# Performance work log

Measured on AMD Instinct MI355X. Metric: run time of the kernel, lower is better.

The kernel has to match this reference:

```python
import math
import jax, jax.numpy as jnp
import numpy as np

N_HEADS = 8
FACTOR = 1


def setup_inputs() -> dict:
    key = jax.random.key(0)
    ks = jax.random.split(key, 8)
    B, L, D = 8, 2048, 512
    scale = 0.05
    return {
        "queries": jax.random.normal(ks[0], (B, L, D), jnp.float32),
        "keys": jax.random.normal(ks[1], (B, L, D), jnp.float32),
        "values": jax.random.normal(ks[2], (B, L, D), jnp.float32),
        "Wq": jax.random.normal(ks[3], (D, D), jnp.float32) * scale,
        "bq": jnp.zeros((D,), jnp.float32),
        "Wk": jax.random.normal(ks[4], (D, D), jnp.float32) * scale,
        "bk": jnp.zeros((D,), jnp.float32),
        "Wv": jax.random.normal(ks[5], (D, D), jnp.float32) * scale,
        "bv": jnp.zeros((D,), jnp.float32),
        "Wo": jax.random.normal(ks[6], (D, D), jnp.float32) * scale,
        "bo": jnp.zeros((D,), jnp.float32),
    }


def _autocorrelation(q, k, v):
    # q,k,v: [B, L, H, E]; L == S assumed (as built in setup_inputs)
    B, L, H, E = q.shape
    qp = jnp.transpose(q, (0, 2, 3, 1))  # [B,H,E,L]
    kp = jnp.transpose(k, (0, 2, 3, 1))
    vp = jnp.transpose(v, (0, 2, 3, 1))
    q_fft = jnp.fft.rfft(qp, axis=-1)
    k_fft = jnp.fft.rfft(kp, axis=-1)
    corr = jnp.fft.irfft(q_fft * jnp.conj(k_fft), n=L, axis=-1)  # [B,H,E,L]

    # training-path time-delay aggregation
    top_k = int(FACTOR * math.log(L))  # static python int
    mean_value = corr.mean(axis=(1, 2))  # [B, L]
    _, index = jax.lax.top_k(mean_value.mean(axis=0), top_k)  # [K] global delays
    weights = mean_value[:, index]  # [B, K]
    tmp_corr = jax.nn.softmax(weights, axis=-1)  # [B, K]
    # roll(v, -d) along last axis == gather at (t + d) mod L
    idx = (jnp.arange(L)[None, :] + index[:, None]) % L  # [K, L]
    patterns = vp[..., idx]  # [B,H,E,K,L]
    delays_agg = jnp.einsum('bhekl,bk->bhel', patterns, tmp_corr)  # [B,H,E,L]
    return jnp.transpose(delays_agg, (0, 3, 1, 2))  # [B,L,H,E]


def reference(queries, keys, values, Wq, bq, Wk, bk, Wv, bv, Wo, bo):
    B, L, Dm = queries.shape
    H = N_HEADS
    q = (queries @ Wq + bq).reshape(B, L, H, -1)
    k = (keys @ Wk + bk).reshape(B, L, H, -1)
    v = (values @ Wv + bv).reshape(B, L, H, -1)
    out = _autocorrelation(q, k, v).reshape(B, L, -1)
    return out @ Wo + bo
```

## Files before the change

kernel.cpp:

```cpp
#include <hip/hip_runtime.h>
#include <stdint.h>

#define BATCH 8
#define L_SEQ 2048
#define D_MODEL 512
#define TOPK 7
#define BM 128
#define BN 128
#define BK 32
#define LT 136

typedef _Float16 f16x8 __attribute__((ext_vector_type(8)));
typedef __attribute__((ext_vector_type(4))) float f32x4;
typedef unsigned short u16;
typedef unsigned int u32;

__device__ __forceinline__ u16 f2h(float f) {
    union { _Float16 h; u16 u; } v; v.h = (_Float16)f; return v.u;
}

__device__ __forceinline__ void load_lds16(const u16* g, u16* l) {
    __builtin_amdgcn_global_load_lds(
        (const __attribute__((address_space(1))) u32*)(g),
        (__attribute__((address_space(3))) u32*)(l), 16, 0, 0);
}


__global__ __launch_bounds__(256, 3) void gemm_qkv(
    const float* __restrict__ Xq, const float* __restrict__ Xk, const float* __restrict__ Xv,
    const u16* __restrict__ Wqt, const u16* __restrict__ Wkt, const u16* __restrict__ Wvt,
    const float* __restrict__ bq, const float* __restrict__ bk, const float* __restrict__ bv,
    u16* __restrict__ QT, u16* __restrict__ KT, u16* __restrict__ Vout)
{
    __shared__ __align__(16) u16 smem[2 * BM * 32 + 2 * BN * BK];
    u16* lT = smem;
    u16* lBb = smem + 2 * BM * 32;

    const int tid = threadIdx.x;
    const int hw = blockIdx.x;
    const int lg = (hw & 7) * 192 + (hw >> 3);
    const int bn = lg & 3, bm = (lg >> 2) & 127, z = lg >> 9;

    const int lane = tid & 63, wave = tid >> 6;
    const int wm = wave >> 1, wn = wave & 1;
    const int l15 = lane & 15, quad = lane >> 4;

    const float* A  = (z == 0) ? Xq  : (z == 1) ? Xk  : Xv;
    const u16*   Bt = (z == 0) ? Wqt : (z == 1) ? Wkt : Wvt;
    const float* bias = (z == 0) ? bq : (z == 1) ? bk : bv;

    const int s0 = wave * 64 + lane, s1 = s0 + 256;
    const int r0 = s0 >> 2, c0 = (s0 & 3) ^ ((r0 >> 1) & 3);
    const int r1 = s1 >> 2, c1 = (s1 & 3) ^ ((r1 >> 1) & 3);
    const u16* gB0 = Bt + (long)(bn * BN + r0) * D_MODEL + c0 * 8;
    const u16* gB1 = Bt + (long)(bn * BN + r1) * D_MODEL + c1 * 8;

    f32x4 acc[4][4] = {};

    {
        load_lds16(gB0, lBb + wave * 512);
        load_lds16(gB1, lBb + 2048 + wave * 512);
        gB0 += BK; gB1 += BK;
        #pragma unroll
        for (int j = 0; j < 4; ++j) {
            int idx = tid + j * 256;
            int row = idx >> 3, c4 = (idx & 7) * 4;
            int cs = (((c4 >> 3) ^ (row & 3)) << 3) | (c4 & 7);
            float4 va = *(const float4*)(A + (long)(bm * BM + row) * D_MODEL + c4);
            ushort4 pa;
            pa.x = f2h(va.x); pa.y = f2h(va.y); pa.z = f2h(va.z); pa.w = f2h(va.w);
            *(ushort4*)&smem[row * 32 + cs] = pa;
        }
    }
    __syncthreads();

    for (int t = 0; t < 16; ++t) {
        const int cur = t & 1;
        u16* lAc = smem + cur * (BM * 32);
        u16* lBc = lBb + cur * (BN * BK);
        u16* lAn = smem + (cur ^ 1) * (BM * 32);
        u16* lBn = lBb + (cur ^ 1) * (BN * BK);
        const bool nx = (t < 15);
        const int k1 = (t + 1) * BK;

        float4 va[4];
        if (nx) {
            load_lds16(gB0, lBn + wave * 512);
            load_lds16(gB1, lBn + 2048 + wave * 512);
            gB0 += BK; gB1 += BK;
            #pragma unroll
            for (int j = 0; j < 4; ++j) {
                int idx = tid + j * 256;
                int row = idx >> 3, c4 = (idx & 7) * 4;
                va[j] = *(const float4*)(A + (long)(bm * BM + row) * D_MODEL + k1 + c4);
            }
        }

        f16x8 fa[4], fb[4];
        #pragma unroll
        for (int i = 0; i < 4; ++i) {
            int r = wm * 64 + i * 16 + l15;
            fa[i] = *(const f16x8*)&lAc[r * 32 + ((quad ^ (r & 3)) << 3)];
        }
        #pragma unroll
        for (int j = 0; j < 4; ++j) {
            int n = wn * 64 + j * 16 + l15;
            int cs = quad ^ ((n >> 1) & 3);
            fb[j] = *(const f16x8*)&lBc[n * 32 + cs * 8];
        }
        #pragma unroll
        for (int i = 0; i < 4; ++i)
            #pragma unroll
            for (int j = 0; j < 4; ++j)
                acc[i][j] = __builtin_amdgcn_mfma_f32_16x16x32_f16(fa[i], fb[j], acc[i][j], 0, 0, 0);

        if (nx) {
            #pragma unroll
            for (int j = 0; j < 4; ++j) {
                int idx = tid + j * 256;
                int row = idx >> 3, c4 = (idx & 7) * 4;
                int cs = (((c4 >> 3) ^ (row & 3)) << 3) | (c4 & 7);
                ushort4 pa;
                pa.x = f2h(va[j].x); pa.y = f2h(va[j].y);
                pa.z = f2h(va[j].z); pa.w = f2h(va[j].w);
                *(ushort4*)&lAn[row * 32 + cs] = pa;
            }
        }
        __syncthreads();
    }

    if (z < 2) {
        u16* out = (z == 0) ? QT : KT;
        const int t0 = (bm * BM) & (L_SEQ - 1);
        const int bb = (bm * BM) >> 11;
        #pragma unroll
        for (int h = 0; h < 2; ++h) {
            __syncthreads();
            if (wn == h) {
                #pragma unroll
                for (int j = 0; j < 4; ++j) {
                    int dloc = j * 16 + l15;
                    float bvv = bias[bn * BN + h * 64 + dloc];
                    #pragma unroll
                    for (int i = 0; i < 4; ++i) {
                        int trow = wm * 64 + i * 16 + quad * 4;
                        #pragma unroll
                        for (int r = 0; r < 4; ++r)
                            lT[dloc * LT + trow + r] = f2h(acc[i][j][r] + bvv);
                    }
                }
            }
            __syncthreads();
            int dloc = tid >> 2, q4 = tid & 3;
            long base = ((long)(bb * D_MODEL + bn * BN + h * 64 + dloc)) * L_SEQ + t0;
            #pragma unroll
            for (int s = 0; s < 4; ++s) {
                int c = q4 * 4 + s;
                *(uint4*)(out + base + c * 8) = *(const uint4*)&lT[dloc * LT + c * 8];
            }
        }
    } else {
        #pragma unroll
        for (int i = 0; i < 4; ++i) {
            int row = bm * BM + wm * 64 + i * 16 + quad * 4;
            #pragma unroll
            for (int j = 0; j < 4; ++j) {
                int col = bn * BN + wn * 64 + j * 16 + l15;
                float bvv = bias[col];
                #pragma unroll
                for (int r = 0; r < 4; ++r)
                    Vout[(long)(row + r) * D_MODEL + col] = f2h(acc[i][j][r] + bvv);
            }
        }
    }
}

__global__ __launch_bounds__(256, 3) void gemm_out_fused(
    const u16* __restrict__ V, const u16* __restrict__ Bt,
    const int* __restrict__ selIdx, const float* __restrict__ selW,
    const float* __restrict__ bias, float* __restrict__ Cp)
{
    __shared__ __align__(16) u16 lA[2 * BM * 32];
    __shared__ __align__(16) u16 lB[2 * BN * BK];

    const int tid = threadIdx.x;
    const int hw = blockIdx.x;
    const int lg = (hw & 7) * 64 + (hw >> 3);
    const int bn = lg & 3, bm = lg >> 2;

    const int lane = tid & 63, wave = tid >> 6;
    const int wm = wave >> 1, wn = wave & 1;
    const int l15 = lane & 15, quad = lane >> 4;

    int   sik[TOPK];
    #pragma unroll
    for (int k = 0; k < TOPK; ++k) sik[k] = selIdx[k];

    const int s0 = wave * 64 + lane, s1 = s0 + 256;
    const int r0 = s0 >> 2, c0 = (s0 & 3) ^ ((r0 >> 1) & 3);
    const int r1 = s1 >> 2, c1 = (s1 & 3) ^ ((r1 >> 1) & 3);
    const u16* gB0 = Bt + (long)(bn * BN + r0) * D_MODEL + c0 * 8;
    const u16* gB1 = Bt + (long)(bn * BN + r1) * D_MODEL + c1 * 8;

    const int row_a = tid >> 2,          c8_a = (tid & 3) * 8;
    const int row_b = (tid + 256) >> 2,  c8_b = (tid & 3) * 8;
    const int csa = ((c8_a >> 3) ^ (row_a & 3)) << 3;
    const int csb = ((c8_b >> 3) ^ (row_b & 3)) << 3;
    const int gra = bm * BM + row_a, grb = bm * BM + row_b;
    const int ba = gra >> 11, la = gra & (L_SEQ - 1);
    const int bb = grb >> 11, lb = grb & (L_SEQ - 1);

    float swa[TOPK], swb[TOPK];
    #pragma unroll
    for (int k = 0; k < TOPK; ++k) {
        swa[k] = selW[ba * TOPK + k];
        swb[k] = selW[bb * TOPK + k];
    }

    union U8 { uint4 u; _Float16 h[8]; };

    f32x4 acc[4][4] = {};

    {
        load_lds16(gB0, lB + wave * 512);
        load_lds16(gB1, lB + 2048 + wave * 512);
        gB0 += BK; gB1 += BK;
        {
            float a[8] = {0,0,0,0,0,0,0,0};
            #pragma unroll
            for (int k = 0; k < TOPK; ++k) {
                int src = (la + sik[k]) & (L_SEQ - 1);
                U8 x; x.u = *(const uint4*)(V + ((long)ba * L_SEQ + src) * D_MODEL + c8_a);
                #pragma unroll
                for (int q = 0; q < 8; ++q) a[q] += swa[k] * (float)x.h[q];
            }
            union { uint4 u; u16 s[8]; } o;
            #pragma unroll
            for (int q = 0; q < 8; ++q) o.s[q] = f2h(a[q]);
            *(uint4*)&lA[row_a * 32 + csa] = o.u;
        }
        {
            float a[8] = {0,0,0,0,0,0,0,0};
            #pragma unroll
            for (int k = 0; k < TOPK; ++k) {
                int src = (lb + sik[k]) & (L_SEQ - 1);
                U8 x; x.u = *(const uint4*)(V + ((long)bb * L_SEQ + src) * D_MODEL + c8_b);
                #pragma unroll
                for (int q = 0; q < 8; ++q) a[q] += swb[k] * (float)x.h[q];
            }
            union { uint4 u; u16 s[8]; } o;
            #pragma unroll
            for (int q = 0; q < 8; ++q) o.s[q] = f2h(a[q]);
            *(uint4*)&lA[row_b * 32 + csb] = o.u;
        }
    }
    __syncthreads();

    for (int t = 0; t < 16; ++t) {
        const int cur = t & 1;
        u16* lAc = lA + cur * (BM * 32);
        u16* lBc = lB + cur * (BN * BK);
        u16* lAn = lA + (cur ^ 1) * (BM * 32);
        u16* lBn = lB + (cur ^ 1) * (BN * BK);
        const bool nx = (t < 15);
        const int k1 = (t + 1) * BK;

        U8 xv[7];
        if (nx) {
            load_lds16(gB0, lBn + wave * 512);
            load_lds16(gB1, lBn + 2048 + wave * 512);
            gB0 += BK; gB1 += BK;
            #pragma unroll
            for (int k = 0; k < TOPK; ++k) {
                int src = (la + sik[k]) & (L_SEQ - 1);
                xv[k].u = *(const uint4*)(V + ((long)ba * L_SEQ + src) * D_MODEL + k1 + c8_a);
            }
        }

        f16x8 fa[4], fb[4];
        #pragma unroll
        for (int i = 0; i < 4; ++i) {
            int r = wm * 64 + i * 16 + l15;
            fa[i] = *(const f16x8*)&lAc[r * 32 + ((quad ^ (r & 3)) << 3)];
        }
        #pragma unroll
        for (int j = 0; j < 4; ++j) {
            int n = wn * 64 + j * 16 + l15;
            int cs = quad ^ ((n >> 1) & 3);
            fb[j] = *(const f16x8*)&lBc[n * 32 + cs * 8];
        }

        #pragma unroll
        for (int i = 0; i < 2; ++i)
            #pragma unroll
            for (int j = 0; j < 4; ++j)
                acc[i][j] = __builtin_amdgcn_mfma_f32_16x16x32_f16(fa[i], fb[j], acc[i][j], 0, 0, 0);

        U8 xw[7];
        if (nx) {
            float a[8] = {0,0,0,0,0,0,0,0};
            #pragma unroll
            for (int k = 0; k < TOPK; ++k) {
                #pragma unroll
                for (int q = 0; q < 8; ++q) a[q] += swa[k] * (float)xv[k].h[q];
            }
            union { uint4 u; u16 s[8]; } o;
            #pragma unroll
            for (int q = 0; q < 8; ++q) o.s[q] = f2h(a[q]);
            *(uint4*)&lAn[row_a * 32 + csa] = o.u;
            #pragma unroll
            for (int k = 0; k < TOPK; ++k) {
                int src = (lb + sik[k]) & (L_SEQ - 1);
                xw[k].u = *(const uint4*)(V + ((long)bb * L_SEQ + src) * D_MODEL + k1 + c8_b);
            }
        }

        #pragma unroll
        for (int i = 2; i < 4; ++i)
            #pragma unroll
            for (int j = 0; j < 4; ++j)
                acc[i][j] = __builtin_amdgcn_mfma_f32_16x16x32_f16(fa[i], fb[j], acc[i][j], 0, 0, 0);

        if (nx) {
            float a[8] = {0,0,0,0,0,0,0,0};
            #pragma unroll
            for (int k = 0; k < TOPK; ++k) {
                #pragma unroll
                for (int q = 0; q < 8; ++q) a[q] += swb[k] * (float)xw[k].h[q];
            }
            union { uint4 u; u16 s[8]; } o;
            #pragma unroll
            for (int q = 0; q < 8; ++q) o.s[q] = f2h(a[q]);
            *(uint4*)&lAn[row_b * 32 + csb] = o.u;
        }
        __syncthreads();
    }

    #pragma unroll
    for (int i = 0; i < 4; ++i) {
        int row = bm * BM + wm * 64 + i * 16 + quad * 4;
        #pragma unroll
        for (int j = 0; j < 4; ++j) {
            int col = bn * BN + wn * 64 + j * 16 + l15;
            float bvv = bias[col];
            #pragma unroll
            for (int r = 0; r < 4; ++r)
                Cp[(long)(row + r) * D_MODEL + col] = acc[i][j][r] + bvv;
        }
    }
}

__device__ __forceinline__ void fft2048_lds(
    float* Zr, float* Zi, const float* Twr, const float* Twi, int tid)
{
    #pragma unroll
    for (int s = 0; s < 10; s += 2) {
        #pragma unroll
        for (int u = 0; u < 2; ++u) {
            int idx = tid + u * 256;
            int d1 = 1 << s;
            int pos = idx & (d1 - 1);
            int i0 = ((idx >> s) << (s + 2)) + pos;
            float w1r = Twr[pos << (10 - s)], w1i = Twi[pos << (10 - s)];
            float w2r = Twr[pos << (9 - s)],  w2i = Twi[pos << (9 - s)];
            int p2 = pos + d1;
            float w3r = Twr[p2 << (9 - s)],   w3i = Twi[p2 << (9 - s)];
            float ar = Zr[i0],          ai = Zi[i0];
            float br = Zr[i0 + d1],     bi = Zi[i0 + d1];
            float cr = Zr[i0 + 2 * d1], ci = Zi[i0 + 2 * d1];
            float dr = Zr[i0 + 3 * d1], di = Zi[i0 + 3 * d1];
            float t1r = br * w1r - bi * w1i, t1i = br * w1i + bi * w1r;
            float Ar = ar + t1r, Ai = ai + t1i, Br = ar - t1r, Bi = ai - t1i;
            float t2r = dr * w1r - di * w1i, t2i = dr * w1i + di * w1r;
            float Cr = cr + t2r, Ci = ci + t2i, Dr = cr - t2r, Di = ci - t2i;
            float u1r = Cr * w2r - Ci * w2i, u1i = Cr * w2i + Ci * w2r;
            float u2r = Dr * w3r - Di * w3i, u2i = Dr * w3i + Di * w3r;
            Zr[i0]          = Ar + u1r; Zi[i0]          = Ai + u1i;
            Zr[i0 + 2 * d1] = Ar - u1r; Zi[i0 + 2 * d1] = Ai - u1i;
            Zr[i0 + d1]     = Br + u2r; Zi[i0 + d1]     = Bi + u2i;
            Zr[i0 + 3 * d1] = Br - u2r; Zi[i0 + 3 * d1] = Bi - u2i;
        }
        __syncthreads();
    }
    #pragma unroll
    for (int j = 0; j < 4; ++j) {
        int idx = tid + j * 256;
        float wr = Twr[idx], wi = Twi[idx];
        float ar = Zr[idx], ai = Zi[idx];
        float br = Zr[idx + 1024], bi = Zi[idx + 1024];
        float tr = br * wr - bi * wi, ti = br * wi + bi * wr;
        Zr[idx] = ar + tr; Zi[idx] = ai + ti;
        Zr[idx + 1024] = ar - tr; Zi[idx + 1024] = ai - ti;
    }
    __syncthreads();
}

__global__ __launch_bounds__(256) void fft_corr_fwd(
    const u16* __restrict__ QT, const u16* __restrict__ KT, float* __restrict__ S)
{
    __shared__ float Zr[2048], Zi[2048];
    __shared__ float Twr[1024], Twi[1024];
    const int tid = threadIdx.x;
    const int b = blockIdx.x >> 7, dg = blockIdx.x & 127;

    #pragma unroll
    for (int j = 0; j < 4; ++j) {
        int i = tid + j * 256;
        float ang = -6.28318530717958647692f * (float)i * (1.0f / 2048.0f);
        float sn, cs; __sincosf(ang, &sn, &cs);
        Twr[i] = cs; Twi[i] = sn;
    }

    float sr[8] = {0,0,0,0,0,0,0,0};
    float si8[8] = {0,0,0,0,0,0,0,0};

    for (int g = 0; g < 4; ++g) {
        int d = dg * 4 + g;
        const u16* qrow = QT + ((long)b * D_MODEL + d) * L_SEQ;
        const u16* krow = KT + ((long)b * D_MODEL + d) * L_SEQ;
        __syncthreads();
        union { uint4 u; _Float16 h[8]; } xq, xk;
        xq.u = *(const uint4*)(qrow + tid * 8);
        xk.u = *(const uint4*)(krow + tid * 8);
        #pragma unroll
        for (int j = 0; j < 8; ++j) {
            int t = tid * 8 + j;
            int tr = (int)(__brev((unsigned)t) >> 21);
            Zr[tr] = (float)xq.h[j];
            Zi[tr] = (float)xk.h[j];
        }
        __syncthreads();
        fft2048_lds(Zr, Zi, Twr, Twi, tid);
        #pragma unroll
        for (int j = 0; j < 8; ++j) {
            int f = tid + j * 256;
            int fm = (2048 - f) & 2047;
            float Xr = Zr[f], Xi = Zi[f], Xmr = Zr[fm], Xmi = Zi[fm];
            float qr = 0.5f * (Xr + Xmr), qi = 0.5f * (Xi - Xmi);
            float dr = Xr - Xmr,          di = Xi + Xmi;
            float kr = 0.5f * di,         ki = -0.5f * dr;
            sr[j]  += qr * kr + qi * ki;
            si8[j] += qi * kr - qr * ki;
        }
    }
    #pragma unroll
    for (int j = 0; j < 8; ++j) {
        int f = tid + j * 256;
        atomicAdd(&S[((long)b * 2048 + f) * 2 + 0], sr[j]);
        atomicAdd(&S[((long)b * 2048 + f) * 2 + 1], si8[j]);
    }
}

__global__ __launch_bounds__(256) void fft_corr_inv(
    const float* __restrict__ S, float* __restrict__ raw)
{
    __shared__ float Zr[2048], Zi[2048];
    __shared__ float Twr[1024], Twi[1024];
    const int tid = threadIdx.x;
    const int b = blockIdx.x;

    #pragma unroll
    for (int j = 0; j < 4; ++j) {
        int i = tid + j * 256;
        float ang = 6.28318530717958647692f * (float)i * (1.0f / 2048.0f);
        float sn, cs; __sincosf(ang, &sn, &cs);
        Twr[i] = cs; Twi[i] = sn;
    }
    #pragma unroll
    for (int j = 0; j < 8; ++j) {
        int f = tid + j * 256;
        int fr = (int)(__brev((unsigned)f) >> 21);
        Zr[fr] = S[((long)b * 2048 + f) * 2 + 0];
        Zi[fr] = S[((long)b * 2048 + f) * 2 + 1];
    }
    __syncthreads();
    fft2048_lds(Zr, Zi, Twr, Twi, tid);
    #pragma unroll
    for (int j = 0; j < 8; ++j) {
        int t = tid + j * 256;
        raw[(long)b * 2048 + t] = Zr[t] * (1.0f / 2048.0f);
    }
}

__global__ __launch_bounds__(256) void transposeW4(
    const float* __restrict__ Wq, const float* __restrict__ Wk,
    const float* __restrict__ Wv, const float* __restrict__ Wo, u16* __restrict__ dstBase)
{
    __shared__ float t[32][33];
    const int z = blockIdx.z;
    const float* src = (z == 0) ? Wq : (z == 1) ? Wk : (z == 2) ? Wv : Wo;
    u16* dst = dstBase + (long)z * D_MODEL * D_MODEL;
    int tx = threadIdx.x & 31, ty = threadIdx.x >> 5;
    int c0 = blockIdx.x * 32, r0 = blockIdx.y * 32;
    #pragma unroll
    for (int r = ty; r < 32; r += 8)
        t[r][tx] = src[(long)(r0 + r) * D_MODEL + c0 + tx];
    __syncthreads();
    #pragma unroll
    for (int r = ty; r < 32; r += 8)
        dst[(long)(c0 + r) * D_MODEL + r0 + tx] = f2h(t[tx][r]);
}

__global__ __launch_bounds__(256) void select_topk(
    const float* __restrict__ raw, int* __restrict__ selIdx, float* __restrict__ selW)
{
    __shared__ float g[L_SEQ];
    __shared__ float wv[4];
    __shared__ int   wi[4];
    __shared__ int   sidx[TOPK];
    __shared__ float wbuf[BATCH][TOPK];
    int tid = threadIdx.x;
    int lane = tid & 63, wave = tid >> 6;
    for (int t = tid; t < L_SEQ; t += 256) {
        float s = 0.0f;
        #pragma unroll
        for (int b = 0; b < BATCH; ++b) s += raw[b * L_SEQ + t];
        g[t] = s;
    }
    __syncthreads();
    for (int it = 0; it < TOPK; ++it) {
        float best = -1e30f; int bi = 0x7fffffff;
        #pragma unroll
        for (int j = 0; j < 8; ++j) {
            int t = tid + j * 256;
            float v = g[t];
            if (v > best || (v == best && t < bi)) { best = v; bi = t; }
        }
        #pragma unroll
        for (int s = 32; s > 0; s >>= 1) {
            float v2 = __shfl_xor(best, s);
            int   i2 = __shfl_xor(bi, s);
            if (v2 > best || (v2 == best && i2 < bi)) { best = v2; bi = i2; }
        }
        if (lane == 0) { wv[wave] = best; wi[wave] = bi; }
        __syncthreads();
        if (tid == 0) {
            float b0 = wv[0]; int i0 = wi[0];
            #pragma unroll
            for (int w = 1; w < 4; ++w)
                if (wv[w] > b0 || (wv[w] == b0 && wi[w] < i0)) { b0 = wv[w]; i0 = wi[w]; }
            sidx[it] = i0; g[i0] = -1e30f;
        }
        __syncthreads();
    }
    if (tid < BATCH * TOPK) {
        int b = tid / TOPK, k = tid % TOPK;
        wbuf[b][k] = raw[b * L_SEQ + sidx[k]] * (1.0f / 512.0f);
    }
    __syncthreads();
    if (tid < BATCH) {
        float mx = -1e30f;
        #pragma unroll
        for (int k = 0; k < TOPK; ++k) mx = fmaxf(mx, wbuf[tid][k]);
        float e[TOPK]; float sum = 0.0f;
        #pragma unroll
        for (int k = 0; k < TOPK; ++k) { e[k] = expf(wbuf[tid][k] - mx); sum += e[k]; }
        #pragma unroll
        for (int k = 0; k < TOPK; ++k) selW[tid * TOPK + k] = e[k] / sum;
    }
    if (tid < TOPK) selIdx[tid] = sidx[tid];
}

extern "C" void kernel_launch(void* const* d_in, const int* in_sizes, int n_in,
                              void* d_out, int out_size, void* d_ws, size_t ws_size,
                              hipStream_t stream)
{
    (void)in_sizes; (void)n_in; (void)out_size; (void)ws_size;
    const float* Xq = (const float*)d_in[0];
    const float* Xk = (const float*)d_in[1];
    const float* Xv = (const float*)d_in[2];
    const float* Wq = (const float*)d_in[3];
    const float* bq = (const float*)d_in[4];
    const float* Wk = (const float*)d_in[5];
    const float* bk = (const float*)d_in[6];
    const float* Wv = (const float*)d_in[7];
    const float* bv = (const float*)d_in[8];
    const float* Wo = (const float*)d_in[9];
    const float* bo = (const float*)d_in[10];

    char* ws = (char*)d_ws;
    const long SLABH = (long)BATCH * L_SEQ * D_MODEL * sizeof(u16);
    u16* QT   = (u16*)(ws);
    u16* KT   = (u16*)(ws + SLABH);
    u16* Vf   = (u16*)(ws + 2 * SLABH);
    const long WSZ = (long)D_MODEL * D_MODEL;
    u16* Wt   = (u16*)(ws + 3 * SLABH);
    u16* Wqt = Wt + 0 * WSZ; u16* Wkt = Wt + 1 * WSZ;
    u16* Wvt = Wt + 2 * WSZ; u16* Wot = Wt + 3 * WSZ;
    float* S   = (float*)(ws + 3 * SLABH + 4 * WSZ * sizeof(u16));
    float* raw = S + (long)BATCH * L_SEQ * 2;
    int*   sIdx = (int*)(raw + (long)BATCH * L_SEQ);
    float* sW   = (float*)(sIdx + 8);

    dim3 tb(256);
    transposeW4<<<dim3(16, 16, 4), tb, 0, stream>>>(Wq, Wk, Wv, Wo, Wt);
    hipMemsetAsync(S, 0, (long)BATCH * L_SEQ * 2 * sizeof(float), stream);

    gemm_qkv<<<dim3(1536), tb, 0, stream>>>(Xq, Xk, Xv, Wqt, Wkt, Wvt, bq, bk, bv, QT, KT, Vf);

    fft_corr_fwd<<<dim3(1024), tb, 0, stream>>>(QT, KT, S);
    fft_corr_inv<<<dim3(BATCH), tb, 0, stream>>>(S, raw);
    select_topk<<<1, tb, 0, stream>>>(raw, sIdx, sW);

    gemm_out_fused<<<dim3(512), tb, 0, stream>>>(Vf, Wot, sIdx, sW, bo, (float*)d_out);
}
```

Measured before the change: 332.6 us.

## Stream fp32 activations directly to LDS and replace atomic FFT reduction with partial buffers

The QKV GEMM now copies fp32 activation tiles straight into LDS with global_load_lds and an XOR swizzle, then converts them to fp16 while building MFMA fragments. This removes the register round-trip and the separate convert-and-store step, at the cost of doubling the A-tile LDS footprint. The forward FFT-correlation kernel now writes per-block partial spectra to a workspace buffer instead of issuing atomicAdds. A new reduce kernel sums those partials, which also removes the memset but adds a launch and 8 MB of extra traffic.

New measurement: 336.5 us. About the same (+1.2%).

```diff
diff --git a/kernel.cpp b/kernel.cpp
--- a/kernel.cpp
+++ b/kernel.cpp
@@ -25,16 +25,15 @@
         (__attribute__((address_space(3))) u32*)(l), 16, 0, 0);
 }
 
-
 __global__ __launch_bounds__(256, 3) void gemm_qkv(
     const float* __restrict__ Xq, const float* __restrict__ Xk, const float* __restrict__ Xv,
     const u16* __restrict__ Wqt, const u16* __restrict__ Wkt, const u16* __restrict__ Wvt,
     const float* __restrict__ bq, const float* __restrict__ bk, const float* __restrict__ bv,
     u16* __restrict__ QT, u16* __restrict__ KT, u16* __restrict__ Vout)
 {
-    __shared__ __align__(16) u16 smem[2 * BM * 32 + 2 * BN * BK];
+    __shared__ __align__(16) u16 smem[2 * 8192 + 2 * 4096];
     u16* lT = smem;
-    u16* lBb = smem + 2 * BM * 32;
+    u16* lBb = smem + 16384;
 
     const int tid = threadIdx.x;
     const int hw = blockIdx.x;
@@ -55,6 +54,15 @@
     const u16* gB0 = Bt + (long)(bn * BN + r0) * D_MODEL + c0 * 8;
     const u16* gB1 = Bt + (long)(bn * BN + r1) * D_MODEL + c1 * 8;
 
+    const float* gA[4];
+    #pragma unroll
+    for (int j = 0; j < 4; ++j) {
+        int id = j * 256 + tid;
+        int r = id >> 3, cp = id & 7;
+        int c = cp ^ (r & 7);
+        gA[j] = A + (long)(bm * BM + r) * D_MODEL + c * 4;
+    }
+
     f32x4 acc[4][4] = {};
 
     {
@@ -62,45 +70,38 @@
         load_lds16(gB1, lBb + 2048 + wave * 512);
         gB0 += BK; gB1 += BK;
         #pragma unroll
-        for (int j = 0; j < 4; ++j) {
-            int idx = tid + j * 256;
-            int row = idx >> 3, c4 = (idx & 7) * 4;
-            int cs = (((c4 >> 3) ^ (row & 3)) << 3) | (c4 & 7);
-            float4 va = *(const float4*)(A + (long)(bm * BM + row) * D_MODEL + c4);
-            ushort4 pa;
-            pa.x = f2h(va.x); pa.y = f2h(va.y); pa.z = f2h(va.z); pa.w = f2h(va.w);
-            *(ushort4*)&smem[row * 32 + cs] = pa;
-        }
+        for (int j = 0; j < 4; ++j)
+            load_lds16((const u16*)gA[j], smem + j * 2048 + wave * 512);
     }
     __syncthreads();
 
     for (int t = 0; t < 16; ++t) {
         const int cur = t & 1;
-        u16* lAc = smem + cur * (BM * 32);
-        u16* lBc = lBb + cur * (BN * BK);
-        u16* lAn = smem + (cur ^ 1) * (BM * 32);
-        u16* lBn = lBb + (cur ^ 1) * (BN * BK);
-        const bool nx = (t < 15);
-        const int k1 = (t + 1) * BK;
-
-        float4 va[4];
-        if (nx) {
-            load_lds16(gB0, lBn + wave * 512);
-            load_lds16(gB1, lBn + 2048 + wave * 512);
+        const float* lAc = (const float*)(smem) + cur * 4096;
+        const u16*   lBc = lBb + cur * 4096;
+
+        if (t < 15) {
+            u16* dstA = smem + (cur ^ 1) * 8192;
+            u16* dstB = lBb + (cur ^ 1) * 4096;
+            load_lds16(gB0, dstB + wave * 512);
+            load_lds16(gB1, dstB + 2048 + wave * 512);
             gB0 += BK; gB1 += BK;
             #pragma unroll
-            for (int j = 0; j < 4; ++j) {
-                int idx = tid + j * 256;
-                int row = idx >> 3, c4 = (idx & 7) * 4;
-                va[j] = *(const float4*)(A + (long)(bm * BM + row) * D_MODEL + k1 + c4);
-            }
+            for (int j = 0; j < 4; ++j)
+                load_lds16((const u16*)(gA[j] + (t + 1) * BK), dstA + j * 2048 + wave * 512);
         }
 
         f16x8 fa[4], fb[4];
         #pragma unroll
         for (int i = 0; i < 4; ++i) {
             int r = wm * 64 + i * 16 + l15;
-            fa[i] = *(const f16x8*)&lAc[r * 32 + ((quad ^ (r & 3)) << 3)];
+            int c0p = (2 * quad) ^ (r & 7);
+            float4 pa = *(const float4*)(lAc + r * 32 + c0p * 4);
+            float4 pb = *(const float4*)(lAc + r * 32 + (c0p ^ 1) * 4);
+            fa[i][0] = (_Float16)pa.x; fa[i][1] = (_Float16)pa.y;
+            fa[i][2] = (_Float16)pa.z; fa[i][3] = (_Float16)pa.w;
+            fa[i][4] = (_Float16)pb.x; fa[i][5] = (_Float16)pb.y;
+            fa[i][6] = (_Float16)pb.z; fa[i][7] = (_Float16)pb.w;
         }
         #pragma unroll
         for (int j = 0; j < 4; ++j) {
@@ -114,18 +115,6 @@
             for (int j = 0; j < 4; ++j)
                 acc[i][j] = __builtin_amdgcn_mfma_f32_16x16x32_f16(fa[i], fb[j], acc[i][j], 0, 0, 0);
 
-        if (nx) {
-            #pragma unroll
-            for (int j = 0; j < 4; ++j) {
-                int idx = tid + j * 256;
-                int row = idx >> 3, c4 = (idx & 7) * 4;
-                int cs = (((c4 >> 3) ^ (row & 3)) << 3) | (c4 & 7);
-                ushort4 pa;
-                pa.x = f2h(va[j].x); pa.y = f2h(va[j].y);
-                pa.z = f2h(va[j].z); pa.w = f2h(va[j].w);
-                *(ushort4*)&lAn[row * 32 + cs] = pa;
-            }
-        }
         __syncthreads();
     }
 
@@ -396,7 +385,7 @@
 }
 
 __global__ __launch_bounds__(256) void fft_corr_fwd(
-    const u16* __restrict__ QT, const u16* __restrict__ KT, float* __restrict__ S)
+    const u16* __restrict__ QT, const u16* __restrict__ KT, float* __restrict__ P)
 {
     __shared__ float Zr[2048], Zi[2048];
     __shared__ float Twr[1024], Twi[1024];
@@ -443,12 +432,28 @@
             si8[j] += qi * kr - qr * ki;
         }
     }
+    float* Pb = P + ((long)(b * 128 + dg) * 2048) * 2;
     #pragma unroll
     for (int j = 0; j < 8; ++j) {
         int f = tid + j * 256;
-        atomicAdd(&S[((long)b * 2048 + f) * 2 + 0], sr[j]);
-        atomicAdd(&S[((long)b * 2048 + f) * 2 + 1], si8[j]);
-    }
+        float2 v; v.x = sr[j]; v.y = si8[j];
+        *(float2*)(Pb + (long)f * 2) = v;
+    }
+}
+
+__global__ __launch_bounds__(256) void fft_reduce(
+    const float* __restrict__ P, float* __restrict__ S)
+{
+    const int b = blockIdx.x >> 3, fc = blockIdx.x & 7;
+    const int f = fc * 256 + threadIdx.x;
+    const float* base = P + ((long)b * 128 * 2048 + f) * 2;
+    float sr = 0.f, si = 0.f;
+    for (int dg = 0; dg < 128; ++dg) {
+        float2 v = *(const float2*)(base + (long)dg * 4096);
+        sr += v.x; si += v.y;
+    }
+    float2 o; o.x = sr; o.y = si;
+    *(float2*)(S + ((long)b * 2048 + f) * 2) = o;
 }
 
 __global__ __launch_bounds__(256) void fft_corr_inv(
@@ -591,14 +596,15 @@
     float* raw = S + (long)BATCH * L_SEQ * 2;
     int*   sIdx = (int*)(raw + (long)BATCH * L_SEQ);
     float* sW   = (float*)(sIdx + 8);
+    float* P    = (float*)(sW + 64);
 
     dim3 tb(256);
     transposeW4<<<dim3(16, 16, 4), tb, 0, stream>>>(Wq, Wk, Wv, Wo, Wt);
-    hipMemsetAsync(S, 0, (long)BATCH * L_SEQ * 2 * sizeof(float), stream);
 
     gemm_qkv<<<dim3(1536), tb, 0, stream>>>(Xq, Xk, Xv, Wqt, Wkt, Wvt, bq, bk, bv, QT, KT, Vf);
 
-    fft_corr_fwd<<<dim3(1024), tb, 0, stream>>>(QT, KT, S);
+    fft_corr_fwd<<<dim3(1024), tb, 0, stream>>>(QT, KT, P);
+    fft_reduce<<<dim3(64), tb, 0, stream>>>(P, S);
     fft_corr_inv<<<dim3(BATCH), tb, 0, stream>>>(S, raw);
     select_topk<<<1, tb, 0, stream>>>(raw, sIdx, sW);
 
```
